# Performance work log

Measured on AMD Instinct MI355X. Metric: run time of the kernel, lower is better.

Reference implementation:

```python
import jax, jax.numpy as jnp
import numpy as np

N_HEADS = 4
N_HIDDEN = 256  # out_features with concat=False
SLOPE = 0.1
NEG_INF = -9e15


def setup_inputs() -> dict:
    key = jax.random.key(0)
    k1, k2, k3, k4 = jax.random.split(key, 4)
    N, F_IN = 4096, 512
    h = jax.random.normal(k1, (N, F_IN), dtype=jnp.float32)
    adj_mat = jax.random.randint(k2, (N, N), 0, 2, dtype=jnp.int32)
    # xavier_normal gain=1.414
    W = jax.random.normal(k3, (F_IN, N_HIDDEN * N_HEADS), dtype=jnp.float32) * (
        1.414 * np.sqrt(2.0 / (F_IN + N_HIDDEN * N_HEADS)))
    a = jax.random.normal(k4, (N_HEADS, 2 * N_HIDDEN, 1), dtype=jnp.float32) * (
        1.414 * np.sqrt(2.0 / (2 * N_HIDDEN + 1)))
    return {"h": h, "adj_mat": adj_mat, "W": W, "a": a}


def reference(h, adj_mat, W, a):
    N = h.shape[0]
    # [N, H*D] -> [H, N, D]
    ht = (h @ W).reshape(N, N_HEADS, N_HIDDEN).transpose(1, 0, 2)
    lr = jax.nn.leaky_relu(ht, SLOPE)
    # additive attention: a split into source/target halves
    src = jnp.einsum('hnd,hd->hn', lr, a[:, :N_HIDDEN, 0])   # [H, N]
    tgt = jnp.einsum('hnd,hd->hn', lr, a[:, N_HIDDEN:, 0])   # [H, N]
    e = src[:, :, None] + tgt[:, None, :]                    # [H, N, N]
    e = jnp.where(adj_mat > 0, e, NEG_INF)
    attn = jax.nn.softmax(e, axis=-1)
    out = jnp.einsum('hnm,hmd->hnd', attn, ht)               # [H, N, D]
    return out.mean(axis=0)                                  # concat=False -> mean over heads
```

## Files before the change

kernel.cpp:

```cpp
#include <hip/hip_runtime.h>

#define N_NODES 4096
#define F_IN 512
#define NHID 256
#define HD 1024
#define NPAD 1152

typedef _Float16 half8 __attribute__((ext_vector_type(8)));
typedef _Float16 half4 __attribute__((ext_vector_type(4)));
typedef float floatx4 __attribute__((ext_vector_type(4)));
typedef float float4v __attribute__((ext_vector_type(4)));
typedef int int4v __attribute__((ext_vector_type(4)));
typedef unsigned int uint4v __attribute__((ext_vector_type(4)));

__device__ __forceinline__ float bf2f(unsigned short u) {
  union { unsigned int i; float f; } x; x.i = ((unsigned int)u) << 16; return x.f;
}

__device__ __forceinline__ void async_copy16(const void* g, void* l) {
  __builtin_amdgcn_global_load_lds((const __attribute__((address_space(1))) void*)g,
                                   (__attribute__((address_space(3))) void*)l, 16, 0, 0);
}

__global__ void detect_kernel(const unsigned short* __restrict__ hbits, int* __restrict__ flag) {
  const int t = threadIdx.x;
  int cnt = 0;
  for (int i = t; i < 1024; i += 256) {
    int e = (hbits[i] >> 7) & 0xFF;
    cnt += (e >= 115 && e <= 135) ? 1 : 0;
  }
  __shared__ int red[256];
  red[t] = cnt; __syncthreads();
  for (int s = 128; s > 0; s >>= 1) { if (t < s) red[t] += red[t + s]; __syncthreads(); }
  if (t == 0) flag[0] = (red[0] >= 900) ? 1 : 0;
}

template <typename OutT>
__device__ __forceinline__ void gemm_core(
    const _Float16* __restrict__ A, const _Float16* __restrict__ BT,
    OutT* __restrict__ C, int K, int ldc, int klen, long csz,
    int lin, int nbx, int nby, int total,
    _Float16* __restrict__ sA, _Float16* __restrict__ sB)
{
  int tile = ((total & 7) == 0) ? ((lin & 7) * (total >> 3) + (lin >> 3)) : lin;
  const int n_idx = tile % nbx;
  const int rem   = tile / nbx;
  const int m_idx = rem % nby;
  const int kz    = rem / nby;

  const int n0 = n_idx * 128;
  const int m0 = m_idx * 128;
  const int kbeg = kz * klen;
  OutT* Cz = C + (long)kz * csz;

  const int t = threadIdx.x;
  const int w = t >> 6;
  const int lane = t & 63;
  const int wm = (w >> 1) << 6;
  const int wn = (w & 1) << 6;

  floatx4 acc[4][4] = {};

  const int l4 = lane >> 2;
  const int kk = (lane & 3) << 3;
  const int c0 = w << 1;

  const _Float16* gA = A + (long)m0 * K;
  const _Float16* gBT = BT + (long)n0 * K;

  const int koff = (lane >> 4) << 3;
  const int rA = wm + (lane & 15);
  const int rB = wn + (lane & 15);

  const int nt = klen >> 5;

  auto STAGE = [&](int buf, int k0) {
#pragma unroll
    for (int p = 0; p < 2; ++p) {
      const int c = c0 + p;
      const int row = c * 16 + l4;
      async_copy16(gA + (long)row * K + k0 + kk, &sA[buf * 4096 + c * 512 + lane * 8]);
      async_copy16(gBT + (long)row * K + k0 + kk, &sB[buf * 4096 + c * 512 + lane * 8]);
    }
  };

  STAGE(0, kbeg);
  if (nt > 1) STAGE(1, kbeg + 32);

  int cur = 0;
  for (int it = 0; it < nt; ++it) {
    const int k0 = kbeg + it * 32;

    if (it + 1 < nt) asm volatile("s_waitcnt vmcnt(4)" ::: "memory");
    else             asm volatile("s_waitcnt vmcnt(0)" ::: "memory");
    __builtin_amdgcn_s_barrier();

    half8 af[4], bf[4];
#pragma unroll
    for (int i = 0; i < 4; ++i)
      af[i] = *(const half8*)&sA[cur * 4096 + (rA + i * 16) * 32 + koff];
#pragma unroll
    for (int i = 0; i < 4; ++i)
      bf[i] = *(const half8*)&sB[cur * 4096 + (rB + i * 16) * 32 + koff];

    asm volatile("s_waitcnt lgkmcnt(0)" ::: "memory");
    __builtin_amdgcn_sched_barrier(0);

    const int nxt = (cur + 2 >= 3) ? cur - 1 : cur + 2;
    if (it + 2 < nt) STAGE(nxt, k0 + 64);

#pragma unroll
    for (int i = 0; i < 4; ++i)
#pragma unroll
      for (int j = 0; j < 4; ++j)
        acc[i][j] = __builtin_amdgcn_mfma_f32_16x16x32_f16(af[i], bf[j], acc[i][j], 0, 0, 0);

    cur = (cur + 1 >= 3) ? 0 : cur + 1;
  }

  const int q4 = (lane >> 4) << 2;
#pragma unroll
  for (int i = 0; i < 4; ++i) {
#pragma unroll
    for (int j = 0; j < 4; ++j) {
      const int gr = m0 + wm + i * 16 + q4;
      const int gc = n0 + wn + j * 16 + (lane & 15);
#pragma unroll
      for (int r = 0; r < 4; ++r)
        Cz[(long)(gr + r) * ldc + gc] = (OutT)acc[i][j][r];
    }
  }
}

template <typename OutT>
__global__ __launch_bounds__(256) void gemm_bt(
    const _Float16* __restrict__ A, const _Float16* __restrict__ BT,
    OutT* __restrict__ C, int K, int ldc, int klen, long csz)
{
  __shared__ _Float16 sA[3 * 128 * 32];
  __shared__ _Float16 sB[3 * 128 * 32];
  const int nbx = gridDim.x, nby = gridDim.y;
  const int total = nbx * nby * gridDim.z;
  const int lin = blockIdx.x + nbx * (blockIdx.y + nby * blockIdx.z);
  gemm_core<OutT>(A, BT, C, K, ldc, klen, csz, lin, nbx, nby, total, sA, sB);
}

__global__ __launch_bounds__(256) void fused_ht_cvt_kernel(
    const _Float16* __restrict__ hF, const _Float16* __restrict__ WT,
    _Float16* __restrict__ ht, const int* __restrict__ adj,
    _Float16* __restrict__ adjF)
{
  __shared__ _Float16 sA[3 * 128 * 32];
  __shared__ _Float16 sB[3 * 128 * 32];
  const int b = blockIdx.x;
  if (b < 256) {
    gemm_core<_Float16>(hF, WT, ht, F_IN, HD, F_IN, 0, b, 8, 32, 256, sA, sB);
  } else {
    const int i = (b - 256) * 256 + threadIdx.x;
    int4v A = ((const int4v*)adj)[2 * i];
    int4v B = ((const int4v*)adj)[2 * i + 1];
    half8 o;
#pragma unroll
    for (int e = 0; e < 4; ++e) {
      o[e]     = (_Float16)(A[e] > 0 ? 1.0f : 0.0f);
      o[4 + e] = (_Float16)(B[e] > 0 ? 1.0f : 0.0f);
    }
    ((half8*)adjF)[i] = o;
  }
}

__global__ void cvt_h_kernel(const void* __restrict__ in, _Float16* __restrict__ out,
                             const int* __restrict__ flag, int n8) {
  int i = blockIdx.x * 256 + threadIdx.x;
  if (i >= n8) return;
  half8 o;
  if (*flag) {
    union { uint4v v; unsigned short s[8]; } u;
    u.v = ((const uint4v*)in)[i];
#pragma unroll
    for (int e = 0; e < 8; ++e) o[e] = (_Float16)bf2f(u.s[e]);
  } else {
    const float4v* f = (const float4v*)in + 2 * i;
    float4v x0 = f[0], x1 = f[1];
#pragma unroll
    for (int e = 0; e < 4; ++e) { o[e] = (_Float16)x0[e]; o[4 + e] = (_Float16)x1[e]; }
  }
  ((half8*)out)[i] = o;
}

__global__ void cvt_a_kernel(const void* __restrict__ a, float* __restrict__ aF,
                             const int* __restrict__ flag) {
  const int t = threadIdx.x;
  const int bf = *flag;
#pragma unroll
  for (int e = 0; e < 8; ++e) {
    int idx = t * 8 + e;
    aF[idx] = bf ? bf2f(((const unsigned short*)a)[idx]) : ((const float*)a)[idx];
  }
}

__global__ void transpose_w_kernel(const void* __restrict__ W, _Float16* __restrict__ WT,
                                   const int* __restrict__ flag) {
  __shared__ _Float16 tile[64][72];
  const int k0 = blockIdx.x * 64, n0 = blockIdx.y * 64;
  const int t = threadIdx.x, r = t >> 3, c = t & 7;
  const int bf = *flag;
#pragma unroll
  for (int q = 0; q < 2; ++q) {
    int k = r + q * 32;
    half8 v;
    if (bf) {
      union { uint4v vv; unsigned short s[8]; } u;
      u.vv = *(const uint4v*)&((const unsigned short*)W)[(long)(k0 + k) * HD + n0 + c * 8];
#pragma unroll
      for (int e = 0; e < 8; ++e) v[e] = (_Float16)bf2f(u.s[e]);
    } else {
      const float4v* f = (const float4v*)&((const float*)W)[(long)(k0 + k) * HD + n0 + c * 8];
      float4v x0 = f[0], x1 = f[1];
#pragma unroll
      for (int e = 0; e < 4; ++e) { v[e] = (_Float16)x0[e]; v[4 + e] = (_Float16)x1[e]; }
    }
    *(half8*)&tile[k][c * 8] = v;
  }
  __syncthreads();
#pragma unroll
  for (int q = 0; q < 2; ++q) {
    int n = r + q * 32;
    half8 o;
#pragma unroll
    for (int e = 0; e < 8; ++e) o[e] = tile[c * 8 + e][n];
    *(half8*)&WT[(long)(n0 + n) * F_IN + k0 + c * 8] = o;
  }
}

__global__ void tgt_kernel(const _Float16* __restrict__ ht, const float* __restrict__ aF,
                           float* __restrict__ tgt) {
  const int i = blockIdx.x;
  const int t = threadIdx.x, h = t >> 6, lane = t & 63;
  half4 v = *(const half4*)&ht[(long)i * HD + h * NHID + lane * 4];
  float4v av = *(const float4v*)&aF[h * 512 + NHID + lane * 4];
  float s = 0.f;
#pragma unroll
  for (int e = 0; e < 4; ++e) {
    float x = (float)v[e];
    x = x > 0.f ? x : 0.1f * x;
    s += x * av[e];
  }
#pragma unroll
  for (int o = 32; o > 0; o >>= 1) s += __shfl_down(s, o);
  if (lane == 0) tgt[h * N_NODES + i] = s;
}

__global__ void maxexp_kernel(const float* __restrict__ tgt, float* __restrict__ wbuf,
                              _Float16* __restrict__ VT) {
  const int h = blockIdx.x, t = threadIdx.x;
  const float* row = tgt + h * N_NODES;
  float4v v[4];
  float m = -3.0e38f;
#pragma unroll
  for (int q = 0; q < 4; ++q) {
    v[q] = *(const float4v*)&row[(t + q * 256) * 4];
#pragma unroll
    for (int e = 0; e < 4; ++e) m = fmaxf(m, v[q][e]);
  }
#pragma unroll
  for (int o = 32; o > 0; o >>= 1) m = fmaxf(m, __shfl_down(m, o));
  __shared__ float red[4];
  if ((t & 63) == 0) red[t >> 6] = m;
  __syncthreads();
  m = fmaxf(fmaxf(red[0], red[1]), fmaxf(red[2], red[3]));
#pragma unroll
  for (int q = 0; q < 4; ++q) {
    const int j0 = (t + q * 256) * 4;
    float4v wv;
#pragma unroll
    for (int e = 0; e < 4; ++e) wv[e] = __expf(v[q][e] - m);
    *(float4v*)&wbuf[h * N_NODES + j0] = wv;
    half4 hv;
#pragma unroll
    for (int e = 0; e < 4; ++e) hv[e] = (_Float16)wv[e];
    *(half4*)&VT[(long)(HD + h) * N_NODES + j0] = hv;
  }
}

__global__ void scaled_transpose_kernel(const _Float16* __restrict__ ht, const float* __restrict__ wbuf,
                                        _Float16* __restrict__ VT) {
  __shared__ _Float16 tile[64][72];
  const int j0 = blockIdx.x * 64, n0 = blockIdx.y * 64;
  const int t = threadIdx.x, r = t >> 3, c = t & 7;
#pragma unroll
  for (int q = 0; q < 2; ++q) {
    int j = r + q * 32;
    *(half8*)&tile[j][c * 8] = *(const half8*)&ht[(long)(j0 + j) * HD + n0 + c * 8];
  }
  __syncthreads();
  const int h = n0 >> 8;
  const float* wrow = wbuf + h * N_NODES + j0;
#pragma unroll
  for (int q = 0; q < 2; ++q) {
    int n = r + q * 32;
    half8 o;
#pragma unroll
    for (int e = 0; e < 8; ++e) {
      int j = c * 8 + e;
      o[e] = (_Float16)(wrow[j] * (float)tile[j][n]);
    }
    *(half8*)&VT[(long)(n0 + n) * N_NODES + j0 + c * 8] = o;
  }
}

__global__ void epilogue_kernel(const float* __restrict__ S, float* __restrict__ out, int ns) {
  const int i = blockIdx.x, d = threadIdx.x;
  const long SZ = (long)N_NODES * NPAD;
  float num[4] = {0.f, 0.f, 0.f, 0.f};
  float den[4] = {0.f, 0.f, 0.f, 0.f};
  for (int z = 0; z < ns; ++z) {
    const float* row = S + z * SZ + (long)i * NPAD;
#pragma unroll
    for (int h = 0; h < 4; ++h) {
      num[h] += row[h * NHID + d];
      den[h] += row[HD + h];
    }
  }
  float r = 0.f;
#pragma unroll
  for (int h = 0; h < 4; ++h) r += num[h] / den[h];
  out[(long)i * NHID + d] = 0.25f * r;
}

extern "C" void kernel_launch(void* const* d_in, const int* in_sizes, int n_in,
                              void* d_out, int out_size, void* d_ws, size_t ws_size,
                              hipStream_t stream) {
  const void* h = nullptr; const int* adj = nullptr; const void* W = nullptr; const void* a = nullptr;
  for (int i = 0; i < n_in; ++i) {
    switch (in_sizes[i]) {
      case 2097152:  h   = d_in[i]; break;
      case 16777216: adj = (const int*)d_in[i]; break;
      case 524288:   W   = d_in[i]; break;
      case 2048:     a   = d_in[i]; break;
      default: break;
    }
  }
  float* out = (float*)d_out;

  char* ws = (char*)d_ws;
  const size_t OFF_ADJF = 0;
  const size_t OFF_VT   = 33554432;
  const size_t OFF_TGT  = OFF_VT + 9437184;
  const size_t OFF_WBUF = OFF_TGT + 65536;
  const size_t OFF_M    = OFF_WBUF + 65536;
  const size_t OFF_AF   = OFF_M + 256;
  const size_t OFF_X    = OFF_AF + 8192;
  const size_t SPART    = 18874368;

  int ns = 1;
  if      (ws_size >= OFF_X + 2 * SPART) ns = 2;
  if (ws_size < OFF_X + SPART || !h || !adj || !W || !a) return;

  _Float16* adjF = (_Float16*)(ws + OFF_ADJF);
  _Float16* VT   = (_Float16*)(ws + OFF_VT);
  float*    tgt  = (float*)(ws + OFF_TGT);
  float*    wbuf = (float*)(ws + OFF_WBUF);
  int*      flag = (int*)(ws + OFF_M + 32);
  float*    aF   = (float*)(ws + OFF_AF);
  _Float16* hF = (_Float16*)(ws + OFF_X);
  _Float16* WT = (_Float16*)(ws + OFF_X + 4194304);
  _Float16* ht = (_Float16*)(ws + OFF_X + 5242880);
  float*    S  = (float*)(ws + OFF_X);

  detect_kernel<<<1, 256, 0, stream>>>((const unsigned short*)h, flag);
  cvt_h_kernel<<<1024, 256, 0, stream>>>(h, hF, flag, 262144);
  cvt_a_kernel<<<1, 256, 0, stream>>>(a, aF, flag);
  transpose_w_kernel<<<dim3(8, 16), 256, 0, stream>>>(W, WT, flag);
  fused_ht_cvt_kernel<<<8448, 256, 0, stream>>>(hF, WT, ht, adj, adjF);
  tgt_kernel<<<4096, 256, 0, stream>>>(ht, aF, tgt);
  maxexp_kernel<<<4, 256, 0, stream>>>(tgt, wbuf, VT);
  scaled_transpose_kernel<<<dim3(64, 16), 256, 0, stream>>>(ht, wbuf, VT);
  gemm_bt<float><<<dim3(9, 32, ns), 256, 0, stream>>>(adjF, VT, S, N_NODES, NPAD,
                                                      N_NODES / ns, (long)N_NODES * NPAD);
  epilogue_kernel<<<4096, 256, 0, stream>>>(S, out, ns);
}
```

Measured before the change: 193.2 us.

## Fuse adjacency int-to-half conversion into attention GEMM A-tile loading

Removes the separate pass that converted the int32 adjacency matrix into an fp16 mask buffer. The aggregation GEMM now loads int32 adjacency tiles into registers, clamps and packs them to fp16 ones and zeros, and writes them to LDS inside its software pipeline. The h@W GEMM is launched alone instead of being fused with the conversion. This saves a full write and re-read of the fp16 mask, but the GEMM now reads twice as many bytes per A tile for each column block and uses register-staged loads instead of async LDS copies.

```diff
diff --git a/kernel.cpp b/kernel.cpp
--- a/kernel.cpp
+++ b/kernel.cpp
@@ -90,7 +90,6 @@
   int cur = 0;
   for (int it = 0; it < nt; ++it) {
     const int k0 = kbeg + it * 32;
-
     if (it + 1 < nt) asm volatile("s_waitcnt vmcnt(4)" ::: "memory");
     else             asm volatile("s_waitcnt vmcnt(0)" ::: "memory");
     __builtin_amdgcn_s_barrier();
@@ -145,27 +144,128 @@
   gemm_core<OutT>(A, BT, C, K, ldc, klen, csz, lin, nbx, nby, total, sA, sB);
 }
 
-__global__ __launch_bounds__(256) void fused_ht_cvt_kernel(
-    const _Float16* __restrict__ hF, const _Float16* __restrict__ WT,
-    _Float16* __restrict__ ht, const int* __restrict__ adj,
-    _Float16* __restrict__ adjF)
+__global__ __launch_bounds__(256) void gemm_adj_kernel(
+    const int* __restrict__ adj, const _Float16* __restrict__ BT, float* __restrict__ C,
+    int K, int ldc, int klen, long csz)
 {
   __shared__ _Float16 sA[3 * 128 * 32];
   __shared__ _Float16 sB[3 * 128 * 32];
-  const int b = blockIdx.x;
-  if (b < 256) {
-    gemm_core<_Float16>(hF, WT, ht, F_IN, HD, F_IN, 0, b, 8, 32, 256, sA, sB);
-  } else {
-    const int i = (b - 256) * 256 + threadIdx.x;
-    int4v A = ((const int4v*)adj)[2 * i];
-    int4v B = ((const int4v*)adj)[2 * i + 1];
-    half8 o;
-#pragma unroll
-    for (int e = 0; e < 4; ++e) {
-      o[e]     = (_Float16)(A[e] > 0 ? 1.0f : 0.0f);
-      o[4 + e] = (_Float16)(B[e] > 0 ? 1.0f : 0.0f);
-    }
-    ((half8*)adjF)[i] = o;
+  const int nbx = gridDim.x, nby = gridDim.y;
+  const int total = nbx * nby * gridDim.z;
+  const int lin = blockIdx.x + nbx * (blockIdx.y + nby * blockIdx.z);
+
+  int tile = ((total & 7) == 0) ? ((lin & 7) * (total >> 3) + (lin >> 3)) : lin;
+  const int n_idx = tile % nbx;
+  const int rem   = tile / nbx;
+  const int m_idx = rem % nby;
+  const int kz    = rem / nby;
+
+  const int n0 = n_idx * 128;
+  const int m0 = m_idx * 128;
+  const int kbeg = kz * klen;
+  float* Cz = C + (long)kz * csz;
+
+  const int t = threadIdx.x;
+  const int w = t >> 6;
+  const int lane = t & 63;
+  const int wm = (w >> 1) << 6;
+  const int wn = (w & 1) << 6;
+
+  floatx4 acc[4][4] = {};
+
+  const int l4 = lane >> 2;
+  const int kkB = (lane & 3) << 3;
+  const int c0 = w << 1;
+  const _Float16* gBT = BT + (long)n0 * K;
+
+  const int koff = (lane >> 4) << 3;
+  const int rA = wm + (lane & 15);
+  const int rB = wn + (lane & 15);
+
+  const int rowr = t >> 3;
+  const int colq = t & 7;
+  const int* gA = adj + (long)m0 * K;
+
+  const int nt = klen >> 5;
+
+  int4v ar[4];
+  auto LOAD_A = [&](int k0) {
+#pragma unroll
+    for (int p = 0; p < 4; ++p)
+      ar[p] = *(const int4v*)(gA + (long)(p * 32 + rowr) * K + k0 + colq * 4);
+  };
+  auto WRITE_A = [&](int buf) {
+#pragma unroll
+    for (int p = 0; p < 4; ++p) {
+      unsigned a0 = (unsigned)ar[p][0]; a0 = a0 < 1u ? a0 : 1u;
+      unsigned a1 = (unsigned)ar[p][1]; a1 = a1 < 1u ? a1 : 1u;
+      unsigned a2 = (unsigned)ar[p][2]; a2 = a2 < 1u ? a2 : 1u;
+      unsigned a3 = (unsigned)ar[p][3]; a3 = a3 < 1u ? a3 : 1u;
+      union { unsigned u[2]; half4 h; } pk;
+      pk.u[0] = (a0 + (a1 << 16)) * 0x3C00u;
+      pk.u[1] = (a2 + (a3 << 16)) * 0x3C00u;
+      *(half4*)&sA[buf * 4096 + (p * 32 + rowr) * 32 + colq * 4] = pk.h;
+    }
+  };
+  auto STAGE_B = [&](int buf, int k0) {
+#pragma unroll
+    for (int p = 0; p < 2; ++p) {
+      const int c = c0 + p;
+      const int row = c * 16 + l4;
+      async_copy16(gBT + (long)row * K + k0 + kkB, &sB[buf * 4096 + c * 512 + lane * 8]);
+    }
+  };
+
+  LOAD_A(kbeg);
+  STAGE_B(0, kbeg);
+  asm volatile("s_waitcnt vmcnt(2)" ::: "memory");
+  WRITE_A(0);
+  if (nt > 1) { LOAD_A(kbeg + 32); STAGE_B(1, kbeg + 32); }
+  asm volatile("s_waitcnt lgkmcnt(0)" ::: "memory");
+
+  int cur = 0;
+  for (int it = 0; it < nt; ++it) {
+    const int k0 = kbeg + it * 32;
+    if (it + 1 < nt) asm volatile("s_waitcnt vmcnt(2)" ::: "memory");
+    else             asm volatile("s_waitcnt vmcnt(0)" ::: "memory");
+    __builtin_amdgcn_s_barrier();
+
+    half8 af[4], bf[4];
+#pragma unroll
+    for (int i = 0; i < 4; ++i)
+      af[i] = *(const half8*)&sA[cur * 4096 + (rA + i * 16) * 32 + koff];
+#pragma unroll
+    for (int i = 0; i < 4; ++i)
+      bf[i] = *(const half8*)&sB[cur * 4096 + (rB + i * 16) * 32 + koff];
+
+    const int nx1 = (cur + 1 >= 3) ? 0 : cur + 1;
+    const int nx2 = (cur + 2 >= 3) ? cur - 1 : cur + 2;
+    if (it + 1 < nt) WRITE_A(nx1);
+    if (it + 2 < nt) { LOAD_A(k0 + 64); STAGE_B(nx2, k0 + 64); }
+
+    asm volatile("s_waitcnt lgkmcnt(0)" ::: "memory");
+    __builtin_amdgcn_sched_barrier(0);
+
+#pragma unroll
+    for (int i = 0; i < 4; ++i)
+#pragma unroll
+      for (int j = 0; j < 4; ++j)
+        acc[i][j] = __builtin_amdgcn_mfma_f32_16x16x32_f16(af[i], bf[j], acc[i][j], 0, 0, 0);
+
+    cur = nx1;
+  }
+
+  const int q4 = (lane >> 4) << 2;
+#pragma unroll
+  for (int i = 0; i < 4; ++i) {
+#pragma unroll
+    for (int j = 0; j < 4; ++j) {
+      const int gr = m0 + wm + i * 16 + q4;
+      const int gc = n0 + wn + j * 16 + (lane & 15);
+#pragma unroll
+      for (int r = 0; r < 4; ++r)
+        Cz[(long)(gr + r) * ldc + gc] = acc[i][j][r];
+    }
   }
 }
 
@@ -344,8 +444,7 @@
   float* out = (float*)d_out;
 
   char* ws = (char*)d_ws;
-  const size_t OFF_ADJF = 0;
-  const size_t OFF_VT   = 33554432;
+  const size_t OFF_VT   = 0;
   const size_t OFF_TGT  = OFF_VT + 9437184;
   const size_t OFF_WBUF = OFF_TGT + 65536;
   const size_t OFF_M    = OFF_WBUF + 65536;
@@ -357,7 +456,6 @@
   if      (ws_size >= OFF_X + 2 * SPART) ns = 2;
   if (ws_size < OFF_X + SPART || !h || !adj || !W || !a) return;
 
-  _Float16* adjF = (_Float16*)(ws + OFF_ADJF);
   _Float16* VT   = (_Float16*)(ws + OFF_VT);
   float*    tgt  = (float*)(ws + OFF_TGT);
   float*    wbuf = (float*)(ws + OFF_WBUF);
@@ -372,11 +470,11 @@
   cvt_h_kernel<<<1024, 256, 0, stream>>>(h, hF, flag, 262144);
   cvt_a_kernel<<<1, 256, 0, stream>>>(a, aF, flag);
   transpose_w_kernel<<<dim3(8, 16), 256, 0, stream>>>(W, WT, flag);
-  fused_ht_cvt_kernel<<<8448, 256, 0, stream>>>(hF, WT, ht, adj, adjF);
+  gemm_bt<_Float16><<<dim3(8, 32, 1), 256, 0, stream>>>(hF, WT, ht, F_IN, HD, F_IN, 0);
   tgt_kernel<<<4096, 256, 0, stream>>>(ht, aF, tgt);
   maxexp_kernel<<<4, 256, 0, stream>>>(tgt, wbuf, VT);
   scaled_transpose_kernel<<<dim3(64, 16), 256, 0, stream>>>(ht, wbuf, VT);
-  gemm_bt<float><<<dim3(9, 32, ns), 256, 0, stream>>>(adjF, VT, S, N_NODES, NPAD,
-                                                      N_NODES / ns, (long)N_NODES * NPAD);
+  gemm_adj_kernel<<<dim3(9, 32, ns), 256, 0, stream>>>(adj, VT, S, N_NODES, NPAD,
+                                                       N_NODES / ns, (long)N_NODES * NPAD);
   epilogue_kernel<<<4096, 256, 0, stream>>>(S, out, ns);
 }
```

New measurement: 220.2 us. 1.14x slower.
